# Performance work log

Hardware: AMD Instinct MI355X
Metric: run time of the kernel (lower is better)

Reference implementation:

```python
import jax, jax.numpy as jnp
import numpy as np

THRESHOLD = 0.7


def ternary_dequant(w, threshold=THRESHOLD):
    """Ternary quantize {-1,0,+1} with masked-mean alpha, return ternary*alpha."""
    abs_w = jnp.abs(w)
    delta = threshold * jnp.mean(abs_w)
    ternary = jnp.where(w > delta, 1.0, jnp.where(w < -delta, -1.0, 0.0)).astype(w.dtype)
    nz = ternary != 0
    cnt = jnp.sum(nz)
    # alpha = mean(|w| over nonzero ternary entries); fall back to mean(|w|) if all-zero
    masked_sum = jnp.sum(jnp.where(nz, abs_w, 0.0))
    alpha = jnp.where(cnt > 0, masked_sum / jnp.maximum(cnt, 1).astype(w.dtype), jnp.mean(abs_w))
    return ternary * alpha


def setup_inputs() -> dict:
    key = jax.random.key(0)
    kx, kw, kb = jax.random.split(key, 3)
    B, S, D_IN, D_OUT = 4, 2048, 4096, 4096
    x = jax.random.normal(kx, (B * S, D_IN), dtype=jnp.float32)
    # xavier-uniform-ish init for latent FP32 weights
    limit = np.sqrt(6.0 / (D_IN + D_OUT)).astype(np.float32)
    weight = jax.random.uniform(kw, (D_OUT, D_IN), dtype=jnp.float32, minval=-limit, maxval=limit)
    bias = jax.random.normal(kb, (D_OUT,), dtype=jnp.float32) * 0.02
    return {"x": x, "weight": weight, "bias": bias}


def reference(x, weight, bias):
    q_weight = ternary_dequant(weight)  # (out, in)
    return jnp.matmul(x, q_weight.T) + bias  # (tokens, out)
```

## Files before the change

### kernel.cpp

```cpp
#include <hip/hip_runtime.h>

#define M_DIM 8192
#define N_DIM 4096
#define K_DIM 4096

typedef __attribute__((ext_vector_type(8))) __bf16 bf16x8;
typedef __attribute__((ext_vector_type(4))) __bf16 bf16x4;
typedef __attribute__((ext_vector_type(4))) float floatx4;

__device__ __forceinline__ void async_copy16(const void* g, void* l) {
    __builtin_amdgcn_global_load_lds(
        (const __attribute__((address_space(1))) void*)g,
        (__attribute__((address_space(3))) void*)l,
        16, 0, 0);
}

__device__ __forceinline__ double wave_reduce_d(double v) {
    #pragma unroll
    for (int o = 32; o > 0; o >>= 1) v += __shfl_down(v, o, 64);
    return v;
}
__device__ __forceinline__ unsigned wave_reduce_u(unsigned v) {
    #pragma unroll
    for (int o = 32; o > 0; o >>= 1) v += __shfl_down(v, o, 64);
    return v;
}

__global__ __launch_bounds__(256) void k_abs_sum(const float4* __restrict__ w4,
                                                 double* __restrict__ part, int n4) {
    const int tid = threadIdx.x;
    int idx = blockIdx.x * 256 + tid;
    const int stride = gridDim.x * 256;
    double s = 0.0;
    for (int i = idx; i < n4; i += stride) {
        float4 v = w4[i];
        s += (double)fabsf(v.x) + (double)fabsf(v.y) +
             (double)fabsf(v.z) + (double)fabsf(v.w);
    }
    s = wave_reduce_d(s);
    __shared__ double sm[4];
    if ((tid & 63) == 0) sm[tid >> 6] = s;
    __syncthreads();
    if (tid == 0) part[blockIdx.x] = sm[0] + sm[1] + sm[2] + sm[3];
}

__global__ __launch_bounds__(256) void k_reduce1(const double* __restrict__ part,
                                                 double* __restrict__ scal) {
    const int tid = threadIdx.x;
    double s = 0.0;
    for (int i = tid; i < 1024; i += 256) s += part[i];
    s = wave_reduce_d(s);
    __shared__ double sm[4];
    if ((tid & 63) == 0) sm[tid >> 6] = s;
    __syncthreads();
    if (tid == 0) {
        double total = sm[0] + sm[1] + sm[2] + sm[3];
        double mean = total / (double)((size_t)N_DIM * K_DIM);
        scal[0] = 0.7 * mean;
        scal[1] = mean;
    }
}

__global__ __launch_bounds__(256) void k_quant(const float4* __restrict__ w4,
                                               bf16x4* __restrict__ tern,
                                               const double* __restrict__ scal,
                                               double* __restrict__ pm,
                                               unsigned* __restrict__ pc, int n4) {
    const double delta = scal[0];
    const int tid = threadIdx.x;
    int idx = blockIdx.x * 256 + tid;
    const int stride = gridDim.x * 256;
    double msum = 0.0;
    unsigned cnt = 0;
    for (int i = idx; i < n4; i += stride) {
        float4 v = w4[i];
        float e[4] = {v.x, v.y, v.z, v.w};
        bf16x4 o;
        #pragma unroll
        for (int c = 0; c < 4; ++c) {
            float wv = e[c];
            float t = ((double)wv > delta) ? 1.0f
                    : (((double)wv < -delta) ? -1.0f : 0.0f);
            if (t != 0.0f) { msum += (double)fabsf(wv); cnt++; }
            o[c] = (__bf16)t;
        }
        tern[i] = o;
    }
    msum = wave_reduce_d(msum);
    cnt  = wave_reduce_u(cnt);
    __shared__ double smd[4];
    __shared__ unsigned smu[4];
    if ((tid & 63) == 0) { smd[tid >> 6] = msum; smu[tid >> 6] = cnt; }
    __syncthreads();
    if (tid == 0) {
        pm[blockIdx.x] = smd[0] + smd[1] + smd[2] + smd[3];
        pc[blockIdx.x] = smu[0] + smu[1] + smu[2] + smu[3];
    }
}

__global__ __launch_bounds__(256) void k_reduce2(const double* __restrict__ pm,
                                                 const unsigned* __restrict__ pc,
                                                 double* __restrict__ scal) {
    const int tid = threadIdx.x;
    double s = 0.0; unsigned c = 0;
    for (int i = tid; i < 1024; i += 256) { s += pm[i]; c += pc[i]; }
    s = wave_reduce_d(s);
    c = wave_reduce_u(c);
    __shared__ double smd[4];
    __shared__ unsigned smu[4];
    if ((tid & 63) == 0) { smd[tid >> 6] = s; smu[tid >> 6] = c; }
    __syncthreads();
    if (tid == 0) {
        double ms = smd[0] + smd[1] + smd[2] + smd[3];
        unsigned ct = smu[0] + smu[1] + smu[2] + smu[3];
        scal[2] = (ct > 0) ? (ms / (double)ct) : scal[1];
    }
}

__global__ __launch_bounds__(256) void k_cvt_x(const float4* __restrict__ x4,
                                               bf16x4* __restrict__ xb) {
    int i = blockIdx.x * 256 + threadIdx.x;
    float4 v = x4[i];
    bf16x4 o;
    o[0] = (__bf16)v.x; o[1] = (__bf16)v.y; o[2] = (__bf16)v.z; o[3] = (__bf16)v.w;
    xb[i] = o;
}

__global__ __launch_bounds__(256) void ternary_gemm(
    const __bf16* __restrict__ A,
    const __bf16* __restrict__ B,
    const float*  __restrict__ bias,
    const double* __restrict__ scal,
    float* __restrict__ C)
{
    __shared__ __attribute__((aligned(128))) __bf16 As[128 * 32];
    __shared__ __attribute__((aligned(128))) __bf16 Bs[128 * 32];

    const int tid  = threadIdx.x;
    const int wave = tid >> 6;
    const int lane = tid & 63;
    const int quad = lane >> 4;
    const int l16  = lane & 15;
    const int wr = wave >> 1;
    const int wc = wave & 1;

    const int br = blockIdx.y;
    const int bc = blockIdx.x;

    const int srow = lane >> 2;
    const int scol = (lane & 3) * 8;
    const int c0 = wave * 2;

    const __bf16* gA0 = A + (size_t)(br * 128 + c0 * 16 + srow) * K_DIM + scol;
    const __bf16* gA1 = gA0 + 16 * K_DIM;
    const __bf16* gB0 = B + (size_t)(bc * 128 + c0 * 16 + srow) * K_DIM + scol;
    const __bf16* gB1 = gB0 + 16 * K_DIM;
    __bf16* lA0 = &As[c0 * 512];
    __bf16* lA1 = &As[(c0 + 1) * 512];
    __bf16* lB0 = &Bs[c0 * 512];
    __bf16* lB1 = &Bs[(c0 + 1) * 512];

    floatx4 acc[4][4] = {};

    const int a_off = (wr * 64 + l16) * 32 + quad * 8;
    const int b_off = (wc * 64 + l16) * 32 + quad * 8;

    for (int k0 = 0; k0 < K_DIM; k0 += 32) {
        async_copy16(gA0, lA0);
        async_copy16(gA1, lA1);
        async_copy16(gB0, lB0);
        async_copy16(gB1, lB1);
        gA0 += 32; gA1 += 32; gB0 += 32; gB1 += 32;
        __syncthreads();

        bf16x8 af[4], bfr[4];
        #pragma unroll
        for (int i = 0; i < 4; ++i)
            af[i] = *(const bf16x8*)&As[a_off + i * 16 * 32];
        #pragma unroll
        for (int j = 0; j < 4; ++j)
            bfr[j] = *(const bf16x8*)&Bs[b_off + j * 16 * 32];

        #pragma unroll
        for (int i = 0; i < 4; ++i)
            #pragma unroll
            for (int j = 0; j < 4; ++j)
                acc[i][j] = __builtin_amdgcn_mfma_f32_16x16x32_bf16(
                    af[i], bfr[j], acc[i][j], 0, 0, 0);
        __syncthreads();
    }

    const float alpha = (float)scal[2];
    float bv[4];
    #pragma unroll
    for (int j = 0; j < 4; ++j)
        bv[j] = bias[bc * 128 + wc * 64 + j * 16 + l16];

    #pragma unroll
    for (int i = 0; i < 4; ++i) {
        const int row0 = br * 128 + wr * 64 + i * 16 + quad * 4;
        #pragma unroll
        for (int j = 0; j < 4; ++j) {
            const int col = bc * 128 + wc * 64 + j * 16 + l16;
            #pragma unroll
            for (int r = 0; r < 4; ++r)
                C[(size_t)(row0 + r) * N_DIM + col] = acc[i][j][r] * alpha + bv[j];
        }
    }
}

extern "C" void kernel_launch(void* const* d_in, const int* in_sizes, int n_in,
                              void* d_out, int out_size, void* d_ws, size_t ws_size,
                              hipStream_t stream) {
    const float* x    = (const float*)d_in[0];
    const float* w    = (const float*)d_in[1];
    const float* bias = (const float*)d_in[2];
    float* out = (float*)d_out;

    char* ws = (char*)d_ws;
    double*   d_scal = (double*)ws;
    double*   part1  = (double*)(ws + 64);
    double*   pm     = (double*)(ws + 8256);
    unsigned* pc     = (unsigned*)(ws + 16448);
    __bf16*   xb     = (__bf16*)(ws + 32768);
    __bf16*   tern   = (__bf16*)(ws + 32768 + (size_t)M_DIM * K_DIM * 2);

    const int n4w = (N_DIM * K_DIM) / 4;

    k_abs_sum<<<1024, 256, 0, stream>>>((const float4*)w, part1, n4w);
    k_reduce1<<<1, 256, 0, stream>>>(part1, d_scal);
    k_quant<<<1024, 256, 0, stream>>>((const float4*)w, (bf16x4*)tern, d_scal, pm, pc, n4w);
    k_reduce2<<<1, 256, 0, stream>>>(pm, pc, d_scal);
    k_cvt_x<<<(M_DIM * K_DIM) / 4 / 256, 256, 0, stream>>>((const float4*)x, (bf16x4*)xb);

    dim3 grid(N_DIM / 128, M_DIM / 128);
    ternary_gemm<<<grid, 256, 0, stream>>>(xb, tern, bias, d_scal, out);
}
```

Before: 575.2 us.

## Fuse preprocessing kernels and swizzle GEMM LDS layout to avoid bank conflicts

Merges the abs-sum and x-conversion into one launch, folds the first scalar reduction into every quant block (each block redundantly reduces the 2048 partials), and folds the second reduction into the GEMM epilogue. This cuts the launch count from six to three. It also applies an XOR swizzle to the 16-byte chunks in LDS for both global-to-LDS copies and fragment reads, aimed at reducing LDS bank conflicts in the GEMM. The cost is redundant reduction work in every quant and GEMM block.

```diff
diff --git a/kernel.cpp b/kernel.cpp
--- a/kernel.cpp
+++ b/kernel.cpp
@@ -26,53 +26,63 @@
     return v;
 }
 
-__global__ __launch_bounds__(256) void k_abs_sum(const float4* __restrict__ w4,
-                                                 double* __restrict__ part, int n4) {
+__global__ __launch_bounds__(256) void k_pre(const float4* __restrict__ w4,
+                                             double* __restrict__ part,
+                                             const float4* __restrict__ x4,
+                                             bf16x4* __restrict__ xb) {
     const int tid = threadIdx.x;
-    int idx = blockIdx.x * 256 + tid;
-    const int stride = gridDim.x * 256;
+    if (blockIdx.x < 2048) {
+        int idx = blockIdx.x * 256 + tid;
+        double s = 0.0;
+        #pragma unroll
+        for (int it = 0; it < 8; ++it) {
+            float4 v = w4[idx + it * (2048 * 256)];
+            s += (double)fabsf(v.x) + (double)fabsf(v.y) +
+                 (double)fabsf(v.z) + (double)fabsf(v.w);
+        }
+        s = wave_reduce_d(s);
+        __shared__ double sm[4];
+        if ((tid & 63) == 0) sm[tid >> 6] = s;
+        __syncthreads();
+        if (tid == 0) part[blockIdx.x] = sm[0] + sm[1] + sm[2] + sm[3];
+    } else {
+        int idx = (blockIdx.x - 2048) * 256 + tid;
+        #pragma unroll
+        for (int it = 0; it < 4; ++it) {
+            int i = idx + it * (8192 * 256);
+            float4 v = x4[i];
+            bf16x4 o;
+            o[0] = (__bf16)v.x; o[1] = (__bf16)v.y;
+            o[2] = (__bf16)v.z; o[3] = (__bf16)v.w;
+            xb[i] = o;
+        }
+    }
+}
+
+__global__ __launch_bounds__(256) void k_quant(const float4* __restrict__ w4,
+                                               bf16x4* __restrict__ tern,
+                                               const double* __restrict__ part,
+                                               double* __restrict__ scal,
+                                               double* __restrict__ pm,
+                                               unsigned* __restrict__ pc) {
+    const int tid = threadIdx.x;
     double s = 0.0;
-    for (int i = idx; i < n4; i += stride) {
-        float4 v = w4[i];
-        s += (double)fabsf(v.x) + (double)fabsf(v.y) +
-             (double)fabsf(v.z) + (double)fabsf(v.w);
-    }
+    #pragma unroll
+    for (int i = 0; i < 8; ++i) s += part[tid + i * 256];
     s = wave_reduce_d(s);
     __shared__ double sm[4];
     if ((tid & 63) == 0) sm[tid >> 6] = s;
     __syncthreads();
-    if (tid == 0) part[blockIdx.x] = sm[0] + sm[1] + sm[2] + sm[3];
-}
-
-__global__ __launch_bounds__(256) void k_reduce1(const double* __restrict__ part,
-                                                 double* __restrict__ scal) {
-    const int tid = threadIdx.x;
-    double s = 0.0;
-    for (int i = tid; i < 1024; i += 256) s += part[i];
-    s = wave_reduce_d(s);
-    __shared__ double sm[4];
-    if ((tid & 63) == 0) sm[tid >> 6] = s;
-    __syncthreads();
-    if (tid == 0) {
-        double total = sm[0] + sm[1] + sm[2] + sm[3];
-        double mean = total / (double)((size_t)N_DIM * K_DIM);
-        scal[0] = 0.7 * mean;
-        scal[1] = mean;
-    }
-}
-
-__global__ __launch_bounds__(256) void k_quant(const float4* __restrict__ w4,
-                                               bf16x4* __restrict__ tern,
-                                               const double* __restrict__ scal,
-                                               double* __restrict__ pm,
-                                               unsigned* __restrict__ pc, int n4) {
-    const double delta = scal[0];
-    const int tid = threadIdx.x;
+    const double mean = (sm[0] + sm[1] + sm[2] + sm[3]) * (1.0 / 16777216.0);
+    const double delta = 0.7 * mean;
+    if (blockIdx.x == 0 && tid == 0) scal[0] = mean;
+
     int idx = blockIdx.x * 256 + tid;
-    const int stride = gridDim.x * 256;
     double msum = 0.0;
     unsigned cnt = 0;
-    for (int i = idx; i < n4; i += stride) {
+    #pragma unroll
+    for (int it = 0; it < 8; ++it) {
+        int i = idx + it * (2048 * 256);
         float4 v = w4[i];
         float e[4] = {v.x, v.y, v.z, v.w};
         bf16x4 o;
@@ -98,43 +108,19 @@
     }
 }
 
-__global__ __launch_bounds__(256) void k_reduce2(const double* __restrict__ pm,
-                                                 const unsigned* __restrict__ pc,
-                                                 double* __restrict__ scal) {
-    const int tid = threadIdx.x;
-    double s = 0.0; unsigned c = 0;
-    for (int i = tid; i < 1024; i += 256) { s += pm[i]; c += pc[i]; }
-    s = wave_reduce_d(s);
-    c = wave_reduce_u(c);
-    __shared__ double smd[4];
-    __shared__ unsigned smu[4];
-    if ((tid & 63) == 0) { smd[tid >> 6] = s; smu[tid >> 6] = c; }
-    __syncthreads();
-    if (tid == 0) {
-        double ms = smd[0] + smd[1] + smd[2] + smd[3];
-        unsigned ct = smu[0] + smu[1] + smu[2] + smu[3];
-        scal[2] = (ct > 0) ? (ms / (double)ct) : scal[1];
-    }
-}
-
-__global__ __launch_bounds__(256) void k_cvt_x(const float4* __restrict__ x4,
-                                               bf16x4* __restrict__ xb) {
-    int i = blockIdx.x * 256 + threadIdx.x;
-    float4 v = x4[i];
-    bf16x4 o;
-    o[0] = (__bf16)v.x; o[1] = (__bf16)v.y; o[2] = (__bf16)v.z; o[3] = (__bf16)v.w;
-    xb[i] = o;
-}
-
 __global__ __launch_bounds__(256) void ternary_gemm(
     const __bf16* __restrict__ A,
     const __bf16* __restrict__ B,
     const float*  __restrict__ bias,
     const double* __restrict__ scal,
+    const double* __restrict__ pm,
+    const unsigned* __restrict__ pc,
     float* __restrict__ C)
 {
     __shared__ __attribute__((aligned(128))) __bf16 As[128 * 32];
     __shared__ __attribute__((aligned(128))) __bf16 Bs[128 * 32];
+    __shared__ double smd[4];
+    __shared__ unsigned smu[4];
 
     const int tid  = threadIdx.x;
     const int wave = tid >> 6;
@@ -148,7 +134,7 @@
     const int bc = blockIdx.x;
 
     const int srow = lane >> 2;
-    const int scol = (lane & 3) * 8;
+    const int scol = ((lane & 3) ^ ((srow >> 1) & 3)) * 8;
     const int c0 = wave * 2;
 
     const __bf16* gA0 = A + (size_t)(br * 128 + c0 * 16 + srow) * K_DIM + scol;
@@ -162,8 +148,9 @@
 
     floatx4 acc[4][4] = {};
 
-    const int a_off = (wr * 64 + l16) * 32 + quad * 8;
-    const int b_off = (wc * 64 + l16) * 32 + quad * 8;
+    const int swz = (quad ^ ((l16 >> 1) & 3)) * 8;
+    const int a_off = (wr * 64 + l16) * 32 + swz;
+    const int b_off = (wc * 64 + l16) * 32 + swz;
 
     for (int k0 = 0; k0 < K_DIM; k0 += 32) {
         async_copy16(gA0, lA0);
@@ -176,10 +163,10 @@
         bf16x8 af[4], bfr[4];
         #pragma unroll
         for (int i = 0; i < 4; ++i)
-            af[i] = *(const bf16x8*)&As[a_off + i * 16 * 32];
+            af[i] = *(const bf16x8*)&As[a_off + i * 512];
         #pragma unroll
         for (int j = 0; j < 4; ++j)
-            bfr[j] = *(const bf16x8*)&Bs[b_off + j * 16 * 32];
+            bfr[j] = *(const bf16x8*)&Bs[b_off + j * 512];
 
         #pragma unroll
         for (int i = 0; i < 4; ++i)
@@ -190,7 +177,17 @@
         __syncthreads();
     }
 
-    const float alpha = (float)scal[2];
+    double s = 0.0; unsigned c = 0;
+    #pragma unroll
+    for (int i = 0; i < 8; ++i) { s += pm[tid + i * 256]; c += pc[tid + i * 256]; }
+    s = wave_reduce_d(s);
+    c = wave_reduce_u(c);
+    if ((tid & 63) == 0) { smd[tid >> 6] = s; smu[tid >> 6] = c; }
+    __syncthreads();
+    const double ms = smd[0] + smd[1] + smd[2] + smd[3];
+    const unsigned ct = smu[0] + smu[1] + smu[2] + smu[3];
+    const float alpha = (float)(ct > 0 ? ms / (double)ct : scal[0]);
+
     float bv[4];
     #pragma unroll
     for (int j = 0; j < 4; ++j)
@@ -219,20 +216,15 @@
 
     char* ws = (char*)d_ws;
     double*   d_scal = (double*)ws;
-    double*   part1  = (double*)(ws + 64);
-    double*   pm     = (double*)(ws + 8256);
-    unsigned* pc     = (unsigned*)(ws + 16448);
-    __bf16*   xb     = (__bf16*)(ws + 32768);
-    __bf16*   tern   = (__bf16*)(ws + 32768 + (size_t)M_DIM * K_DIM * 2);
-
-    const int n4w = (N_DIM * K_DIM) / 4;
-
-    k_abs_sum<<<1024, 256, 0, stream>>>((const float4*)w, part1, n4w);
-    k_reduce1<<<1, 256, 0, stream>>>(part1, d_scal);
-    k_quant<<<1024, 256, 0, stream>>>((const float4*)w, (bf16x4*)tern, d_scal, pm, pc, n4w);
-    k_reduce2<<<1, 256, 0, stream>>>(pm, pc, d_scal);
-    k_cvt_x<<<(M_DIM * K_DIM) / 4 / 256, 256, 0, stream>>>((const float4*)x, (bf16x4*)xb);
+    double*   part   = (double*)(ws + 64);
+    double*   pm     = (double*)(ws + 16448);
+    unsigned* pc     = (unsigned*)(ws + 32832);
+    __bf16*   xb     = (__bf16*)(ws + 65536);
+    __bf16*   tern   = (__bf16*)(ws + 65536 + (size_t)M_DIM * K_DIM * 2);
+
+    k_pre<<<10240, 256, 0, stream>>>((const float4*)w, part, (const float4*)x, (bf16x4*)xb);
+    k_quant<<<2048, 256, 0, stream>>>((const float4*)w, (bf16x4*)tern, part, d_scal, pm, pc);
 
     dim3 grid(N_DIM / 128, M_DIM / 128);
-    ternary_gemm<<<grid, 256, 0, stream>>>(xb, tern, bias, d_scal, out);
-}
+    ternary_gemm<<<grid, 256, 0, stream>>>(xb, tern, bias, d_scal, pm, pc, out);
+}
```

New measurement: 578.6 us. About the same (+0.6%).
